# Kernel optimization log

Hardware: AMD Instinct MI355X
Metric: run time of the kernel (lower is better)

Reference implementation:

```python
import jax, jax.numpy as jnp
import numpy as np

N, D, C, K, M = 32768, 512, 64, 16, 128
DEPTH = 4            # log2(K): decision-tree depth per codebook
NODES = K - 1        # 15 internal tree nodes per codebook


def _build_selection_matrix():
    # Node i of the binary tree lives at level log2(i+1) and thresholds the
    # level-l selected dimension of its codebook.
    S = np.zeros((C * NODES, C * DEPTH), dtype=np.float32)
    base = np.zeros((NODES, DEPTH), dtype=np.float32)
    for i in range(NODES):
        base[i, int(np.log2(i + 1))] = 1.0
    for c in range(C):
        S[c * NODES:(c + 1) * NODES, c * DEPTH:(c + 1) * DEPTH] = base
    return S


def _build_bit_matrix():
    # Leaf k scores +1/-1 on each of its DEPTH ancestor nodes; the true leaf
    # attains the maximal score DEPTH.
    base = np.zeros((K, NODES), dtype=np.float32)
    for k in range(K):
        for l in range(DEPTH):
            node = (1 << l) - 1 + (k >> (DEPTH - l))   # ancestor at level l
            bit = (k >> (DEPTH - 1 - l)) & 1            # right(1)/left(0)
            base[k, node] = 1.0 if bit else -1.0
    B = np.zeros((C * K, C * NODES), dtype=np.float32)
    for c in range(C):
        B[c * K:(c + 1) * K, c * NODES:(c + 1) * NODES] = base
    return B


def setup_inputs() -> dict:
    key = jax.random.key(0)
    k1, k2, k3, k4 = jax.random.split(key, 4)
    I = jax.random.normal(k1, (N, D), jnp.float32)
    T = jax.random.normal(k2, (C * NODES,), jnp.float32) * 0.1   # thresholds
    L = jax.random.normal(k3, (M, C, K), jnp.float32)            # LUT
    dims = jnp.sort(jax.random.randint(k4, (C * DEPTH,), 0, D))  # selected cols
    S = jnp.asarray(_build_selection_matrix())
    B = jnp.asarray(_build_bit_matrix())
    temp = jnp.ones((1,), jnp.float32)
    return {"I": I, "T": T, "L": L, "S": S, "B": B, "dims": dims, "temp": temp}


def reference(I, T, L, S, B, dims, temp):
    t = temp[0]
    x_sel = I[:, dims]                                  # (N, C*DEPTH) gather
    h = x_sel @ S.T - T                                 # (N, C*NODES)
    tanh_h = jnp.tanh(h / t)
    # straight-through sign: forward sign(h), backward d(tanh(h/t))
    sign_ste = jnp.sign(h) - jax.lax.stop_gradient(tanh_h) + tanh_h
    b = sign_ste @ B.T                                  # (N, C*K) leaf scores
    soft = jax.nn.softmax(b.reshape(-1, C, K) / t, axis=2)
    hard = jax.nn.one_hot(jnp.argmax(soft, axis=2), K, dtype=soft.dtype)
    # straight-through one-hot encoding E: forward hard, backward soft
    E = hard - jax.lax.stop_gradient(soft) + soft       # (N, C, K)
    return jnp.einsum("nck,mck->nm", E, L)              # LUT gather-sum readout
```

## Files before the change

kernel.cpp:

```cpp
#include <hip/hip_runtime.h>

#define N_TOTAL 32768
#define D_DIM   512
#define C_DIM   64
#define K_DIM   16
#define M_DIM   128
#define NODES_  15
#define ROWS_B  32

typedef unsigned short u16;
typedef unsigned int   u32;
typedef unsigned long long u64;
typedef unsigned char  u8;
typedef float  f32x4   __attribute__((ext_vector_type(4)));
typedef short  short8v __attribute__((ext_vector_type(8)));

#define WAIT_VM(N) asm volatile("s_waitcnt vmcnt(" #N ")" ::: "memory")

__device__ __forceinline__ u32 f2bf_bits(float f) {
    u32 u = __float_as_uint(f);
    return (u + 0x7FFFu + ((u >> 16) & 1u)) >> 16;
}

__device__ __forceinline__ void gload_lds16(const float* g, float* l) {
    __builtin_amdgcn_global_load_lds(
        (const __attribute__((address_space(1))) void*)g,
        (__attribute__((address_space(3))) void*)l, 16, 0, 0);
}

__global__ __launch_bounds__(256) void build_lbf(
    const float* __restrict__ L, u16* __restrict__ Lbf)
{
    int idx  = blockIdx.x * 256 + threadIdx.x;
    int lane = idx & 63;
    int ch   = (idx >> 6) & 31;
    int ct   = idx >> 11;
    int m  = ct * 16 + (lane & 15);
    int k0 = ch * 32 + ((lane >> 4) * 8);
    const float* src = L + (size_t)m * 1024 + k0;
    float4 a = *(const float4*)(src);
    float4 b = *(const float4*)(src + 4);
    u32 w0 = f2bf_bits(a.x) | (f2bf_bits(a.y) << 16);
    u32 w1 = f2bf_bits(a.z) | (f2bf_bits(a.w) << 16);
    u32 w2 = f2bf_bits(b.x) | (f2bf_bits(b.y) << 16);
    u32 w3 = f2bf_bits(b.z) | (f2bf_bits(b.w) << 16);
    *(uint4*)(Lbf + (size_t)idx * 8) = make_uint4(w0, w1, w2, w3);
}

__global__ __launch_bounds__(256, 4) void mega_kernel(
    const float* __restrict__ I,
    const float* __restrict__ T,
    const int* __restrict__ dims,
    const u16* __restrict__ Lbf,
    float* __restrict__ out)
{
    __shared__ float sI[2 * 8 * D_DIM];
    __shared__ float sT[C_DIM * NODES_];
    __shared__ u8    sC2[C_DIM * 36];

    const int tid  = threadIdx.x;
    const int lane = tid & 63;
    const int wv   = tid >> 6;
    const int rowBase = blockIdx.x * ROWS_B;

    const int4 dml = ((const int4*)dims)[lane];

    auto issue = [&](int ci, int buf) {
        const float* src = I + (size_t)(rowBase + ci * 8 + wv * 2) * D_DIM;
        float* dst = sI + buf * 8 * D_DIM + wv * 2 * D_DIM;
        #pragma unroll
        for (int i = 0; i < 4; ++i)
            gload_lds16(src + i * 256 + lane * 4, dst + i * 256);
    };

    u32 c4[2][2] = {{0u, 0u}, {0u, 0u}};
    const float* tc = sT + lane * NODES_;

    auto descend = [&](int buf, int ci) {
        const int rt = ci >> 1, p = ci & 1;
        #pragma unroll
        for (int rr = 0; rr < 2; ++rr) {
            const float* v = sI + buf * 8 * D_DIM + (wv * 2 + rr) * D_DIM;
            float x0 = v[dml.x], x1 = v[dml.y], x2 = v[dml.z], x3 = v[dml.w];
            int node = 0, k = 0;
            int b0 = (x0 - tc[0] > 0.0f) ? 1 : 0;
            k = b0; node = 1 + b0;
            int b1 = (x1 - tc[node] > 0.0f) ? 1 : 0;
            k = (k << 1) | b1; node = (node << 1) + 1 + b1;
            int b2 = (x2 - tc[node] > 0.0f) ? 1 : 0;
            k = (k << 1) | b2; node = (node << 1) + 1 + b2;
            int b3 = (x3 - tc[node] > 0.0f) ? 1 : 0;
            k = (k << 1) | b3;
            c4[rr][p] |= (u32)k << (8 * rt);
        }
    };

    issue(0, 0);
    for (int j = tid; j < C_DIM * NODES_; j += 256) sT[j] = T[j];
    __syncthreads();
    issue(1, 1);

    descend(0, 0);
    issue(2, 0);
    WAIT_VM(4);
    descend(1, 1);
    issue(3, 1);
    WAIT_VM(4);
    descend(0, 2);
    WAIT_VM(0);
    descend(1, 3);

    #pragma unroll
    for (int p = 0; p < 2; ++p)
        #pragma unroll
        for (int rr = 0; rr < 2; ++rr)
            *(u16*)(sC2 + lane * 36 + (p * 8 + wv * 2 + rr) * 2) =
                (u16)c4[rr][p];
    __syncthreads();

    const int l15     = lane & 15;
    const int clsLane = (lane >> 5) & 1;
    const int kb      = ((lane >> 4) & 1) * 8;

    f32x4 acc[2][2] = {};

    const u16* lb0 = Lbf + ((size_t)(wv * 2 + 0) * 32 * 64 + lane) * 8;
    const u16* lb1 = Lbf + ((size_t)(wv * 2 + 1) * 32 * 64 + lane) * 8;

    #pragma unroll 4
    for (int ch = 0; ch < 32; ++ch) {
        union { uint4 u; short8v v; } b0, b1;
        b0.u = *(const uint4*)(lb0 + (size_t)ch * 64 * 8);
        b1.u = *(const uint4*)(lb1 + (size_t)ch * 64 * 8);
        const int cls = ch * 2 + clsLane;
        const u32 codes2 = *(const u16*)(sC2 + cls * 36 + l15 * 2);
        #pragma unroll
        for (int rt = 0; rt < 2; ++rt) {
            u32 cd = (codes2 >> (8 * rt)) & 0xFFu;
            u32 tt = cd - (u32)kb;
            u64 sv = 0x3F80ull << ((tt & 3) * 16);
            union { u64 d[2]; short8v v; } a;
            a.d[0] = (tt < 4) ? sv : 0ull;
            a.d[1] = (tt >= 4 && tt < 8) ? sv : 0ull;
            acc[rt][0] = __builtin_amdgcn_mfma_f32_16x16x32_bf16(
                             a.v, b0.v, acc[rt][0], 0, 0, 0);
            acc[rt][1] = __builtin_amdgcn_mfma_f32_16x16x32_bf16(
                             a.v, b1.v, acc[rt][1], 0, 0, 0);
        }
    }

    #pragma unroll
    for (int rt = 0; rt < 2; ++rt) {
        #pragma unroll
        for (int cj = 0; cj < 2; ++cj) {
            int col = (wv * 2 + cj) * 16 + l15;
            int r0  = rowBase + rt * 16 + ((lane >> 4) << 2);
            float* o = out + (size_t)r0 * M_DIM + col;
            o[0 * M_DIM] = acc[rt][cj][0];
            o[1 * M_DIM] = acc[rt][cj][1];
            o[2 * M_DIM] = acc[rt][cj][2];
            o[3 * M_DIM] = acc[rt][cj][3];
        }
    }
}

extern "C" void kernel_launch(void* const* d_in, const int* in_sizes, int n_in,
                              void* d_out, int out_size, void* d_ws, size_t ws_size,
                              hipStream_t stream) {
    const float* I    = (const float*)d_in[0];
    const float* T    = (const float*)d_in[1];
    const float* L    = (const float*)d_in[2];
    const int*   dims = (const int*)d_in[5];

    u16* Lbf = (u16*)d_ws;

    hipLaunchKernelGGL(build_lbf, dim3(64), dim3(256), 0, stream, L, Lbf);
    hipLaunchKernelGGL(mega_kernel, dim3(N_TOTAL / ROWS_B), dim3(256), 0, stream,
                       I, T, dims, Lbf, (float*)d_out);
}
```

Before: 118.3 us.

## Keep LUT in registers and pipeline descend with MFMA over 16-row sub-tiles

Blocks grow to 512 threads covering 128 rows, and each of the 8 waves keeps its 16-column slice of the bf16 LUT in 32 uint4 registers for the whole block instead of reloading it from global memory every chunk. Rows are processed in 8 sub-tiles of 16 with double-buffered async loads of I, and the tree descent for the next sub-tile overlaps the MFMA readout of the current one. This amortises the LUT reads across more rows and hides the I-load latency, at the cost of much higher register pressure and lower occupancy (2 blocks per CU).

```diff
diff --git a/kernel.cpp b/kernel.cpp
--- a/kernel.cpp
+++ b/kernel.cpp
@@ -3,10 +3,10 @@
 #define N_TOTAL 32768
 #define D_DIM   512
 #define C_DIM   64
-#define K_DIM   16
 #define M_DIM   128
 #define NODES_  15
-#define ROWS_B  32
+#define ROWS_B  128
+#define NSUB    8
 
 typedef unsigned short u16;
 typedef unsigned int   u32;
@@ -20,6 +20,12 @@
 __device__ __forceinline__ u32 f2bf_bits(float f) {
     u32 u = __float_as_uint(f);
     return (u + 0x7FFFu + ((u >> 16) & 1u)) >> 16;
+}
+
+__device__ __forceinline__ void lds_barrier() {
+    asm volatile("s_waitcnt lgkmcnt(0)" ::: "memory");
+    __builtin_amdgcn_s_barrier();
+    asm volatile("" ::: "memory");
 }
 
 __device__ __forceinline__ void gload_lds16(const float* g, float* l) {
@@ -47,16 +53,16 @@
     *(uint4*)(Lbf + (size_t)idx * 8) = make_uint4(w0, w1, w2, w3);
 }
 
-__global__ __launch_bounds__(256, 4) void mega_kernel(
+__global__ __launch_bounds__(512, 2) void mega_kernel(
     const float* __restrict__ I,
     const float* __restrict__ T,
     const int* __restrict__ dims,
     const u16* __restrict__ Lbf,
     float* __restrict__ out)
 {
-    __shared__ float sI[2 * 8 * D_DIM];
+    __shared__ float sI[2][16 * D_DIM];
     __shared__ float sT[C_DIM * NODES_];
-    __shared__ u8    sC2[C_DIM * 36];
+    __shared__ u8    sC[2][C_DIM * 20];
 
     const int tid  = threadIdx.x;
     const int lane = tid & 63;
@@ -65,22 +71,26 @@
 
     const int4 dml = ((const int4*)dims)[lane];
 
-    auto issue = [&](int ci, int buf) {
-        const float* src = I + (size_t)(rowBase + ci * 8 + wv * 2) * D_DIM;
-        float* dst = sI + buf * 8 * D_DIM + wv * 2 * D_DIM;
+    uint4 Breg[32];
+    #pragma unroll
+    for (int ch = 0; ch < 32; ++ch)
+        Breg[ch] = *(const uint4*)(Lbf + ((size_t)(wv * 32 + ch) * 64 + lane) * 8);
+
+    auto issue = [&](int t) {
+        const float* src = I + (size_t)(rowBase + t * 16 + wv * 2) * D_DIM;
+        float* dst = &sI[t & 1][wv * 2 * D_DIM];
         #pragma unroll
         for (int i = 0; i < 4; ++i)
             gload_lds16(src + i * 256 + lane * 4, dst + i * 256);
     };
 
-    u32 c4[2][2] = {{0u, 0u}, {0u, 0u}};
     const float* tc = sT + lane * NODES_;
 
-    auto descend = [&](int buf, int ci) {
-        const int rt = ci >> 1, p = ci & 1;
+    auto descend_write = [&](int t) {
+        u32 pk = 0;
         #pragma unroll
         for (int rr = 0; rr < 2; ++rr) {
-            const float* v = sI + buf * 8 * D_DIM + (wv * 2 + rr) * D_DIM;
+            const float* v = &sI[t & 1][(wv * 2 + rr) * D_DIM];
             float x0 = v[dml.x], x1 = v[dml.y], x2 = v[dml.z], x3 = v[dml.w];
             int node = 0, k = 0;
             int b0 = (x0 - tc[0] > 0.0f) ? 1 : 0;
@@ -91,77 +101,57 @@
             k = (k << 1) | b2; node = (node << 1) + 1 + b2;
             int b3 = (x3 - tc[node] > 0.0f) ? 1 : 0;
             k = (k << 1) | b3;
-            c4[rr][p] |= (u32)k << (8 * rt);
+            pk |= (u32)k << (8 * rr);
         }
+        *(u16*)(&sC[t & 1][lane * 20 + wv * 2]) = (u16)pk;
     };
-
-    issue(0, 0);
-    for (int j = tid; j < C_DIM * NODES_; j += 256) sT[j] = T[j];
-    __syncthreads();
-    issue(1, 1);
-
-    descend(0, 0);
-    issue(2, 0);
-    WAIT_VM(4);
-    descend(1, 1);
-    issue(3, 1);
-    WAIT_VM(4);
-    descend(0, 2);
-    WAIT_VM(0);
-    descend(1, 3);
-
-    #pragma unroll
-    for (int p = 0; p < 2; ++p)
-        #pragma unroll
-        for (int rr = 0; rr < 2; ++rr)
-            *(u16*)(sC2 + lane * 36 + (p * 8 + wv * 2 + rr) * 2) =
-                (u16)c4[rr][p];
-    __syncthreads();
 
     const int l15     = lane & 15;
     const int clsLane = (lane >> 5) & 1;
     const int kb      = ((lane >> 4) & 1) * 8;
 
-    f32x4 acc[2][2] = {};
-
-    const u16* lb0 = Lbf + ((size_t)(wv * 2 + 0) * 32 * 64 + lane) * 8;
-    const u16* lb1 = Lbf + ((size_t)(wv * 2 + 1) * 32 * 64 + lane) * 8;
-
-    #pragma unroll 4
-    for (int ch = 0; ch < 32; ++ch) {
-        union { uint4 u; short8v v; } b0, b1;
-        b0.u = *(const uint4*)(lb0 + (size_t)ch * 64 * 8);
-        b1.u = *(const uint4*)(lb1 + (size_t)ch * 64 * 8);
-        const int cls = ch * 2 + clsLane;
-        const u32 codes2 = *(const u16*)(sC2 + cls * 36 + l15 * 2);
+    auto gemm_store = [&](int t) {
+        f32x4 acc = {0.f, 0.f, 0.f, 0.f};
+        const u8* cb = &sC[t & 1][0];
         #pragma unroll
-        for (int rt = 0; rt < 2; ++rt) {
-            u32 cd = (codes2 >> (8 * rt)) & 0xFFu;
+        for (int ch = 0; ch < 32; ++ch) {
+            const int cls = ch * 2 + clsLane;
+            u32 cd = cb[cls * 20 + l15];
             u32 tt = cd - (u32)kb;
             u64 sv = 0x3F80ull << ((tt & 3) * 16);
             union { u64 d[2]; short8v v; } a;
             a.d[0] = (tt < 4) ? sv : 0ull;
             a.d[1] = (tt >= 4 && tt < 8) ? sv : 0ull;
-            acc[rt][0] = __builtin_amdgcn_mfma_f32_16x16x32_bf16(
-                             a.v, b0.v, acc[rt][0], 0, 0, 0);
-            acc[rt][1] = __builtin_amdgcn_mfma_f32_16x16x32_bf16(
-                             a.v, b1.v, acc[rt][1], 0, 0, 0);
+            union { uint4 u; short8v v; } b;
+            b.u = Breg[ch];
+            acc = __builtin_amdgcn_mfma_f32_16x16x32_bf16(a.v, b.v, acc, 0, 0, 0);
         }
+        int r0 = rowBase + t * 16 + ((lane >> 4) << 2);
+        float* o = out + (size_t)r0 * M_DIM + wv * 16 + l15;
+        o[0 * M_DIM] = acc[0];
+        o[1 * M_DIM] = acc[1];
+        o[2 * M_DIM] = acc[2];
+        o[3 * M_DIM] = acc[3];
+    };
+
+    issue(0); issue(1);
+    for (int j = tid; j < C_DIM * NODES_; j += 512) sT[j] = T[j];
+    __syncthreads();
+    descend_write(0);
+    lds_barrier();
+
+    for (int t = 0; t < NSUB - 1; ++t) {
+        gemm_store(t);
+        if (t < NSUB - 2) {
+            issue(t + 2);
+            WAIT_VM(4);
+        } else {
+            WAIT_VM(0);
+        }
+        descend_write(t + 1);
+        lds_barrier();
     }
-
-    #pragma unroll
-    for (int rt = 0; rt < 2; ++rt) {
-        #pragma unroll
-        for (int cj = 0; cj < 2; ++cj) {
-            int col = (wv * 2 + cj) * 16 + l15;
-            int r0  = rowBase + rt * 16 + ((lane >> 4) << 2);
-            float* o = out + (size_t)r0 * M_DIM + col;
-            o[0 * M_DIM] = acc[rt][cj][0];
-            o[1 * M_DIM] = acc[rt][cj][1];
-            o[2 * M_DIM] = acc[rt][cj][2];
-            o[3 * M_DIM] = acc[rt][cj][3];
-        }
-    }
+    gemm_store(NSUB - 1);
 }
 
 extern "C" void kernel_launch(void* const* d_in, const int* in_sizes, int n_in,
@@ -175,6 +165,6 @@
     u16* Lbf = (u16*)d_ws;
 
     hipLaunchKernelGGL(build_lbf, dim3(64), dim3(256), 0, stream, L, Lbf);
-    hipLaunchKernelGGL(mega_kernel, dim3(N_TOTAL / ROWS_B), dim3(256), 0, stream,
+    hipLaunchKernelGGL(mega_kernel, dim3(N_TOTAL / ROWS_B), dim3(512), 0, stream,
                        I, T, dims, Lbf, (float*)d_out);
 }
```

New measurement: 128.9 us. 9.0% more time.
